# Kernel optimization log

Measured on AMD Instinct MI355X. Metric: run time of the kernel, lower is better.

Reference implementation:

```python
import jax, jax.numpy as jnp
import numpy as np

B, M, D, OUT = 16384, 4096, 512, 128


def setup_inputs() -> dict:
    key = jax.random.key(0)
    ks = jax.random.split(key, 5)
    x = jax.random.normal(ks[0], (B, D), dtype=jnp.float32)
    support = jax.random.normal(ks[1], (M, D), dtype=jnp.float32)
    gamma = jnp.float32(1.0)
    head_w = jax.random.normal(ks[2], (OUT, M), dtype=jnp.float32) / np.sqrt(M)
    head_b = jax.random.normal(ks[3], (OUT,), dtype=jnp.float32) * 0.01
    scale = jnp.ones((1,), dtype=jnp.float32)
    shift = jnp.zeros((1,), dtype=jnp.float32)
    return {"x": x, "support": support, "gamma": gamma,
            "head_w": head_w, "head_b": head_b,
            "scale": scale, "shift": shift}


def reference(x, support, gamma, head_w, head_b, scale, shift):
    x2 = jnp.sum(x * x, axis=-1, keepdims=True)           # [B, 1]
    s2 = jnp.sum(support * support, axis=-1)              # [M]
    xs = jnp.einsum('bd,md->bm', x, support)              # [B, M]
    sqdist = jnp.maximum(x2 + s2[None, :] - 2.0 * xs, 0.0)
    k = jnp.exp(-gamma * sqdist)                          # RBF kernel [B, M]
    out = jnp.einsum('bm,om->bo', k, head_w) + head_b     # linear head [B, OUT]
    return scale * out + shift
```

## Files before the change

### kernel.cpp

```cpp
#include <hip/hip_runtime.h>

typedef unsigned int u32;
typedef unsigned short u16;
typedef unsigned char u8;
typedef __attribute__((ext_vector_type(8))) __bf16 bf16x8;
typedef __attribute__((ext_vector_type(4))) float f32x4;
typedef __attribute__((ext_vector_type(4))) int i32x4;

#define NB 16384
#define NM 4096
#define ND 512
#define NOUT 128
#define L2E 1.44269504088896340736f


#define WAITLG(N) do { asm volatile("s_waitcnt vmcnt(" #N ") lgkmcnt(0)" ::: "memory"); \
                       __builtin_amdgcn_sched_barrier(0); } while (0)
#define LGKM(N) do { asm volatile("s_waitcnt lgkmcnt(" #N ")" ::: "memory"); \
                     __builtin_amdgcn_sched_barrier(0); } while (0)
#define SB0() __builtin_amdgcn_sched_barrier(0)

__device__ __forceinline__ u16 f2bf(float f) {
  u32 u = __float_as_uint(f);
  u += 0x7FFFu + ((u >> 16) & 1u);
  return (u16)(u >> 16);
}

__device__ __forceinline__ u8 f2fp8(float f) {
  u32 u = __float_as_uint(f);
  u32 s = (u >> 24) & 0x80u;
  u32 au = u & 0x7FFFFFFFu;
  if (au < 0x3C800000u) return (u8)s;
  au += 0x000FFFFFu + ((au >> 20) & 1u);
  u32 e = (au >> 23) - 120u;
  u32 m = (au >> 20) & 7u;
  return (u8)(s | (e << 3) | m);
}

__device__ __forceinline__ void stage16(const void* g, void* l) {
  __builtin_amdgcn_global_load_lds((__attribute__((address_space(1))) void*)g,
                                   (__attribute__((address_space(3))) void*)l,
                                   16, 0, 0);
}

__device__ __forceinline__ bf16x8 ldg_b128(const void* p) {
  i32x4 r;
  asm volatile("global_load_dwordx4 %0, %1, off" : "=&v"(r) : "v"(p) : "memory");
  return __builtin_bit_cast(bf16x8, r);
}

__device__ __forceinline__ uint4 pack8bf(float4 v0, float4 v1) {
  uint4 pk;
  pk.x = (u32)f2bf(v0.x) | ((u32)f2bf(v0.y) << 16);
  pk.y = (u32)f2bf(v0.z) | ((u32)f2bf(v0.w) << 16);
  pk.z = (u32)f2bf(v1.x) | ((u32)f2bf(v1.y) << 16);
  pk.w = (u32)f2bf(v1.z) | ((u32)f2bf(v1.w) << 16);
  return pk;
}

__device__ __forceinline__ uint2 pack8f8(float4 v0, float4 v1) {
  uint2 pk;
  pk.x = (u32)f2fp8(v0.x) | ((u32)f2fp8(v0.y) << 8) |
         ((u32)f2fp8(v0.z) << 16) | ((u32)f2fp8(v0.w) << 24);
  pk.y = (u32)f2fp8(v1.x) | ((u32)f2fp8(v1.y) << 8) |
         ((u32)f2fp8(v1.z) << 16) | ((u32)f2fp8(v1.w) << 24);
  return pk;
}

__global__ __launch_bounds__(256) void prep_all(const float* __restrict__ x,
                                                const float* __restrict__ s,
                                                const float* __restrict__ hw,
                                                const float* __restrict__ gamma_p,
                                                u8*  __restrict__ x_ws,
                                                u8*  __restrict__ s_ws,
                                                u16* __restrict__ hw_ws,
                                                float* __restrict__ x2g,
                                                float* __restrict__ s2g,
                                                float* __restrict__ out) {
  __shared__ uint2 t8[2048];
  __shared__ uint4 t16[2048];
  const int tid = threadIdx.x, bid = blockIdx.x;
  const int lane = tid & 63, w = tid >> 6;

  if (bid < 640) {
    const bool isx = bid < 512;
    const int blk = isx ? bid : (bid - 512);
    const float* src_m = isx ? x : s;
    u8*    dst_ws = isx ? x_ws : s_ws;
    float* sq_out = isx ? x2g : s2g;
    const float gl   = gamma_p[0] * L2E;
    const float cmul = isx ? 1.0f : (-2.0f * gl);
    const int big  = isx ? (blk >> 1) : (blk >> 2);
    const int roff = isx ? ((blk & 1) * 32) : ((blk & 3) * 32);
    const int rows = isx ? 64 : 128;

    #pragma unroll
    for (int p = 0; p < 8; ++p) {
      const int row = p * 4 + w;
      const float* src = src_m + (size_t)(blk * 32 + row) * ND + lane * 8;
      float4 v0 = *(const float4*)src;
      float4 v1 = *(const float4*)(src + 4);
      float ss = v0.x*v0.x + v0.y*v0.y + v0.z*v0.z + v0.w*v0.w
               + v1.x*v1.x + v1.y*v1.y + v1.z*v1.z + v1.w*v1.w;
      #pragma unroll
      for (int off = 32; off > 0; off >>= 1) ss += __shfl_down(ss, off);
      if (lane == 0) sq_out[blk * 32 + row] = gl * ss;
      v0.x *= cmul; v0.y *= cmul; v0.z *= cmul; v0.w *= cmul;
      v1.x *= cmul; v1.y *= cmul; v1.z *= cmul; v1.w *= cmul;
      t8[lane * 32 + ((row + lane) & 31)] = pack8f8(v0, v1);
    }
    __syncthreads();
    #pragma unroll
    for (int p = 0; p < 8; ++p) {
      const int kg = p * 8 + (tid >> 5);
      const int row = tid & 31;
      uint2 pk = t8[kg * 32 + ((row + kg) & 31)];
      *(uint2*)&dst_ws[(((size_t)(big * 64 + kg)) * rows + roff + row) * 8] = pk;
    }
  } else if (bid < 672) {
    const int blk = bid - 640;
    #pragma unroll
    for (int p = 0; p < 8; ++p) {
      const int o = p * 16 + (tid >> 4);
      const int kg = tid & 15;
      const float* src = hw + (size_t)o * NM + blk * 128 + kg * 8;
      float4 v0 = *(const float4*)src;
      float4 v1 = *(const float4*)(src + 4);
      t16[o * 16 + ((kg + o) & 15)] = pack8bf(v0, v1);
    }
    __syncthreads();
    #pragma unroll
    for (int it = 0; it < 8; ++it) {
      const int kg = it * 2 + (tid >> 7);
      const int o = tid & 127;
      uint4 pk = t16[o * 16 + ((kg + o) & 15)];
      *(uint4*)&hw_ws[(((size_t)(blk * 16 + kg)) * 128 + o) * 8] = pk;
    }
  } else {
    float4* o4 = (float4*)out;
    const float4 z = {0.f, 0.f, 0.f, 0.f};
    size_t base = (size_t)(bid - 672) * 8192 + tid;
    #pragma unroll 8
    for (int i = 0; i < 32; ++i) o4[base + (size_t)i * 256] = z;
  }
}

__global__ __launch_bounds__(256, 2)
void rbf_fused(const u8* __restrict__ x_ws, const u8* __restrict__ s_ws,
               const u16* __restrict__ hw_ws, const float* __restrict__ x2g,
               const float* __restrict__ s2g, const float* __restrict__ head_b,
               const float* __restrict__ scale_p, const float* __restrict__ shift_p,
               float* __restrict__ out)
{
  extern __shared__ __align__(16) char smem[];

  const int tid  = threadIdx.x;
  const int w    = tid >> 6;
  const int lane = tid & 63;
  const int quad = lane >> 4;
  const int l16  = lane & 15;
  const int wr   = w & 1;
  const int wc   = w >> 1;
  const int xcd  = blockIdx.x & 7;
  const int rb   = (blockIdx.x >> 3) * 2 + (xcd & 1);
  const int half = xcd >> 1;
  const int b0   = rb * 64;

  const float vscale = scale_p[0];
  const float vshift = shift_p[0];

  const u8* xsrc = x_ws + (size_t)rb * 32768;
  const u8* ssrc = s_ws + (size_t)(half * 8) * 65536;

  auto stage_grp = [&](int mt_s, int grp_s) {
    const u8* sp = ssrc + (size_t)mt_s * 65536 + grp_s * 8192;
    char* dp = smem + 32768 + (grp_s & 3) * 8192;
    stage16(sp + tid * 16, dp + tid * 16);
    stage16(sp + 4096 + tid * 16, dp + 4096 + tid * 16);
  };

  f32x4 x2v[2];
  #pragma unroll
  for (int r = 0; r < 2; ++r)
    x2v[r] = *(const f32x4*)&x2g[b0 + wr * 32 + r * 16 + quad * 4];
  SB0();
  #pragma unroll
  for (int i = 0; i < 8; ++i)
    stage16(xsrc + i * 4096 + tid * 16, smem + i * 4096 + tid * 16);
  SB0();
  stage_grp(0, 0); SB0();
  stage_grp(0, 1); SB0();
  stage_grp(0, 2);
  WAITLG(0);
  __builtin_amdgcn_s_barrier();
  SB0();

  long long aF[2][2][2];
  long long bF[2][2][4];
  bf16x8 b2[2][4];
  bf16x8 a2h[4][2];

  #pragma unroll
  for (int k2 = 0; k2 < 2; ++k2) {
    #pragma unroll
    for (int r = 0; r < 2; ++r)
      aF[0][k2][r] = *(const long long*)(smem + ((k2 * 4 + quad) * 64 + wr * 32 + r * 16 + l16) * 8);
    #pragma unroll
    for (int c = 0; c < 4; ++c)
      bF[0][k2][c] = *(const long long*)(smem + 32768 +
                       ((k2 * 4 + quad) * 128 + wc * 64 + c * 16 + l16) * 8);
  }
  LGKM(0);
  __builtin_amdgcn_s_barrier();
  SB0();

  const f32x4 zf = {0.f, 0.f, 0.f, 0.f};
  f32x4 acc_xs[2][4];
  f32x4 acc_out[2][4];
  #pragma unroll
  for (int r = 0; r < 2; ++r)
    #pragma unroll
    for (int c = 0; c < 4; ++c) { acc_xs[r][c] = zf; acc_out[r][c] = zf; }

  #pragma unroll 1
  for (int mt = 0; mt < 8; ++mt) {
    const int mtg = half * 8 + mt;

    if (mt > 0) {
      #pragma unroll
      for (int ks = 0; ks < 4; ++ks) {
        const int kg = ks * 4 + quad;
        #pragma unroll
        for (int r = 0; r < 2; ++r)
          a2h[ks][r] = *(const bf16x8*)(smem + 65536 + (kg * 64 + wr * 32 + r * 16 + l16) * 16);
      }
      LGKM(0);
    }
    float s2v[4];

    #pragma unroll
    for (int grp = 0; grp < 8; ++grp) {
      const int p  = grp & 1;
      const int pn = p ^ 1;
      const int gN = grp + 1;
      const bool doRd = !(mt == 7 && grp == 7);

      if ((grp & 1) == 0) {
        if (grp == 0) {
          #pragma unroll
          for (int c = 0; c < 4; ++c)
            s2v[c] = s2g[mtg * 128 + wc * 64 + c * 16 + l16];
          SB0();
        }
        if (grp == 0)      { stage_grp(mt, 3); stage_grp(mt, 4); }
        else if (grp == 2) { stage_grp(mt, 5); stage_grp(mt, 6); }
        else if (grp == 4) { stage_grp(mt, 7); if (mt < 7) stage_grp(mt + 1, 0); }
        else               { if (mt < 7) { stage_grp(mt + 1, 1); stage_grp(mt + 1, 2); } }
        SB0();
        if ((grp < 6 && mt >= 1) || (grp == 6 && mt <= 6)) {
          const int um = mt + (grp == 6);
          const int ks = ((grp >> 1) + 1) & 3;
          const size_t sb = (size_t)((half * 8 + um - 1) * 16 + ks * 4 + quad);
          #pragma unroll
          for (int c = 0; c < 4; ++c)
            b2[((grp >> 1) + 1) & 1][c] = ldg_b128(hw_ws + (sb * 128 + wc * 64 + c * 16 + l16) * 8);
        }
        SB0();
      }

      __builtin_amdgcn_s_setprio(1);
      #pragma unroll
      for (int r = 0; r < 2; ++r)
        #pragma unroll
        for (int c = 0; c < 4; ++c)
          acc_xs[r][c] = __builtin_amdgcn_mfma_f32_16x16x32_fp8_fp8(
              aF[p][0][r], bF[p][0][c], acc_xs[r][c], 0, 0, 0);
      __builtin_amdgcn_s_setprio(0);
      SB0();
      if (doRd) {
        #pragma unroll
        for (int k2 = 0; k2 < 2; ++k2)
          #pragma unroll
          for (int r = 0; r < 2; ++r)
            aF[pn][k2][r] = *(const long long*)(smem +
                ((((gN & 7) * 2 + k2) * 4 + quad) * 64 + wr * 32 + r * 16 + l16) * 8);
        #pragma unroll
        for (int c = 0; c < 2; ++c)
          bF[pn][0][c] = *(const long long*)(smem + 32768 + (gN & 3) * 8192 +
              ((0 * 4 + quad) * 128 + wc * 64 + c * 16 + l16) * 8);
      }
      SB0();

      __builtin_amdgcn_s_setprio(1);
      #pragma unroll
      for (int r = 0; r < 2; ++r)
        #pragma unroll
        for (int c = 0; c < 4; ++c)
          acc_xs[r][c] = __builtin_amdgcn_mfma_f32_16x16x32_fp8_fp8(
              aF[p][1][r], bF[p][1][c], acc_xs[r][c], 0, 0, 0);
      __builtin_amdgcn_s_setprio(0);
      SB0();
      if (doRd) {
        #pragma unroll
        for (int c = 2; c < 4; ++c)
          bF[pn][0][c] = *(const long long*)(smem + 32768 + (gN & 3) * 8192 +
              ((0 * 4 + quad) * 128 + wc * 64 + c * 16 + l16) * 8);
        #pragma unroll
        for (int c = 0; c < 4; ++c)
          bF[pn][1][c] = *(const long long*)(smem + 32768 + (gN & 3) * 8192 +
              ((1 * 4 + quad) * 128 + wc * 64 + c * 16 + l16) * 8);
      }
      SB0();

      if ((grp & 1) == 0) {
        if (mt > 0) {
          __builtin_amdgcn_s_setprio(1);
          #pragma unroll
          for (int r = 0; r < 2; ++r)
            #pragma unroll
            for (int c = 0; c < 4; ++c)
              acc_out[r][c] = __builtin_amdgcn_mfma_f32_16x16x32_bf16(
                  a2h[grp >> 1][r], b2[(grp >> 1) & 1][c], acc_out[r][c], 0, 0, 0);
          __builtin_amdgcn_s_setprio(0);
        }
        LGKM(0);
      } else {
        WAITLG(0);
        __builtin_amdgcn_s_barrier();
        SB0();
      }
    }

    {
      #pragma unroll
      for (int r = 0; r < 2; ++r)
        #pragma unroll
        for (int c = 0; c < 4; ++c) {
          const int cl = wc * 64 + c * 16 + l16;
          char* kbase = smem + 65536 + (cl >> 3) * 1024 + (cl & 7) * 2;
          #pragma unroll
          for (int i = 0; i < 4; ++i) {
            const int row = wr * 32 + r * 16 + quad * 4 + i;
            const float t = acc_xs[r][c][i] + x2v[r][i] + s2v[c];
            float kv = __builtin_amdgcn_exp2f(-t);
            kv = fminf(kv, 1.0f);
            *(u16*)(kbase + row * 16) = (u16)(__float_as_uint(kv) >> 16);
            acc_xs[r][c][i] = 0.0f;
          }
        }
    }
    LGKM(0);
    __builtin_amdgcn_s_barrier();
    SB0();
  }

  #pragma unroll
  for (int ks = 0; ks < 4; ++ks) {
    const int kg = ks * 4 + quad;
    const size_t sb = (size_t)((half * 8 + 7) * 16 + kg);
    bf16x8 bb[4], aa[2];
    #pragma unroll
    for (int c = 0; c < 4; ++c)
      bb[c] = *(const bf16x8*)(hw_ws + (sb * 128 + wc * 64 + c * 16 + l16) * 8);
    #pragma unroll
    for (int r = 0; r < 2; ++r)
      aa[r] = *(const bf16x8*)(smem + 65536 + (kg * 64 + wr * 32 + r * 16 + l16) * 16);
    #pragma unroll
    for (int r = 0; r < 2; ++r)
      #pragma unroll
      for (int c = 0; c < 4; ++c)
        acc_out[r][c] = __builtin_amdgcn_mfma_f32_16x16x32_bf16(aa[r], bb[c], acc_out[r][c], 0, 0, 0);
  }

  float addv[4];
  #pragma unroll
  for (int c = 0; c < 4; ++c) {
    const int col = wc * 64 + c * 16 + l16;
    addv[c] = (half == 0) ? (vscale * head_b[col] + vshift) : 0.0f;
  }
  #pragma unroll
  for (int r = 0; r < 2; ++r)
    #pragma unroll
    for (int c = 0; c < 4; ++c) {
      const int col = wc * 64 + c * 16 + l16;
      #pragma unroll
      for (int i = 0; i < 4; ++i) {
        const int row = b0 + wr * 32 + r * 16 + quad * 4 + i;
        atomicAdd(&out[(size_t)row * NOUT + col], vscale * acc_out[r][c][i] + addv[c]);
      }
    }
}

extern "C" void kernel_launch(void* const* d_in, const int* in_sizes, int n_in,
                              void* d_out, int out_size, void* d_ws, size_t ws_size,
                              hipStream_t stream) {
  const float* x       = (const float*)d_in[0];
  const float* support = (const float*)d_in[1];
  const float* gamma   = (const float*)d_in[2];
  const float* head_w  = (const float*)d_in[3];
  const float* head_b  = (const float*)d_in[4];
  const float* scale   = (const float*)d_in[5];
  const float* shift   = (const float*)d_in[6];
  float* out = (float*)d_out;

  char* w = (char*)d_ws;
  u8*    x_ws  = (u8*)(w);
  u8*    s_ws  = (u8*)(w + 8388608);
  u16*   hw_ws = (u16*)(w + 10485760);
  float* x2g   = (float*)(w + 11534336);
  float* s2g   = (float*)(w + 11599872);

  static bool lds_init = false;
  if (!lds_init) {
    hipFuncSetAttribute(reinterpret_cast<const void*>(rbf_fused),
                        hipFuncAttributeMaxDynamicSharedMemorySize, 81920);
    lds_init = true;
  }

  prep_all<<<736, 256, 0, stream>>>(x, support, head_w, gamma,
                                    x_ws, s_ws, hw_ws, x2g, s2g, out);
  rbf_fused<<<1024, 256, 81920, stream>>>(x_ws, s_ws, hw_ws, x2g, s2g,
                                          head_b, scale, shift, out);
}
```

Measured before the change: 182.3 us.

## Load x fragments straight from global and shrink LDS to static 48KB

The x tile is no longer staged into LDS. Each wave loads its fp8 A fragments directly from global memory with dwordx2 loads, one group ahead. LDS drops from 80KB dynamic to 48KB static, which could allow more blocks per CU. Support staging now runs one group per iteration, the per-tile bulk read of the kernel matrix is split into per-step reads, and the waitcnt and barrier schedule is retuned to match. The cost is more global load traffic and latency exposed in the inner loop.

Measured after the change: 243.8 us. 1.34x slower.

```diff
diff --git a/kernel.cpp b/kernel.cpp
--- a/kernel.cpp
+++ b/kernel.cpp
@@ -47,6 +47,11 @@
   i32x4 r;
   asm volatile("global_load_dwordx4 %0, %1, off" : "=&v"(r) : "v"(p) : "memory");
   return __builtin_bit_cast(bf16x8, r);
+}
+__device__ __forceinline__ long long ldg_b64(const void* p) {
+  long long r;
+  asm volatile("global_load_dwordx2 %0, %1, off" : "=&v"(r) : "v"(p) : "memory");
+  return r;
 }
 
 __device__ __forceinline__ uint4 pack8bf(float4 v0, float4 v1) {
@@ -152,7 +157,7 @@
                const float* __restrict__ scale_p, const float* __restrict__ shift_p,
                float* __restrict__ out)
 {
-  extern __shared__ __align__(16) char smem[];
+  __shared__ __align__(16) char smem[49152];
 
   const int tid  = threadIdx.x;
   const int w    = tid >> 6;
@@ -172,44 +177,43 @@
   const u8* xsrc = x_ws + (size_t)rb * 32768;
   const u8* ssrc = s_ws + (size_t)(half * 8) * 65536;
 
+  const u8* xb0 = xsrc + quad * 512 + (wr * 32 + l16) * 8;
+  const u8* xb1 = xsrc + quad * 512 + (wr * 32 + 16 + l16) * 8;
+
   auto stage_grp = [&](int mt_s, int grp_s) {
     const u8* sp = ssrc + (size_t)mt_s * 65536 + grp_s * 8192;
-    char* dp = smem + 32768 + (grp_s & 3) * 8192;
+    char* dp = smem + (grp_s & 3) * 8192;
     stage16(sp + tid * 16, dp + tid * 16);
     stage16(sp + 4096 + tid * 16, dp + 4096 + tid * 16);
   };
 
+  long long aF[2][2][2];
+  long long bF[2][2][4];
+  bf16x8 b2[2][4];
+  bf16x8 a2[2];
+
   f32x4 x2v[2];
   #pragma unroll
   for (int r = 0; r < 2; ++r)
     x2v[r] = *(const f32x4*)&x2g[b0 + wr * 32 + r * 16 + quad * 4];
   SB0();
-  #pragma unroll
-  for (int i = 0; i < 8; ++i)
-    stage16(xsrc + i * 4096 + tid * 16, smem + i * 4096 + tid * 16);
-  SB0();
   stage_grp(0, 0); SB0();
   stage_grp(0, 1); SB0();
-  stage_grp(0, 2);
+  stage_grp(0, 2); SB0();
+  aF[0][0][0] = ldg_b64(xb0);
+  aF[0][0][1] = ldg_b64(xb1);
+  aF[0][1][0] = ldg_b64(xb0 + 2048);
+  aF[0][1][1] = ldg_b64(xb1 + 2048);
   WAITLG(0);
   __builtin_amdgcn_s_barrier();
   SB0();
 
-  long long aF[2][2][2];
-  long long bF[2][2][4];
-  bf16x8 b2[2][4];
-  bf16x8 a2h[4][2];
-
-  #pragma unroll
-  for (int k2 = 0; k2 < 2; ++k2) {
-    #pragma unroll
-    for (int r = 0; r < 2; ++r)
-      aF[0][k2][r] = *(const long long*)(smem + ((k2 * 4 + quad) * 64 + wr * 32 + r * 16 + l16) * 8);
+  #pragma unroll
+  for (int k2 = 0; k2 < 2; ++k2)
     #pragma unroll
     for (int c = 0; c < 4; ++c)
-      bF[0][k2][c] = *(const long long*)(smem + 32768 +
+      bF[0][k2][c] = *(const long long*)(smem +
                        ((k2 * 4 + quad) * 128 + wc * 64 + c * 16 + l16) * 8);
-  }
   LGKM(0);
   __builtin_amdgcn_s_barrier();
   SB0();
@@ -225,17 +229,6 @@
   #pragma unroll 1
   for (int mt = 0; mt < 8; ++mt) {
     const int mtg = half * 8 + mt;
-
-    if (mt > 0) {
-      #pragma unroll
-      for (int ks = 0; ks < 4; ++ks) {
-        const int kg = ks * 4 + quad;
-        #pragma unroll
-        for (int r = 0; r < 2; ++r)
-          a2h[ks][r] = *(const bf16x8*)(smem + 65536 + (kg * 64 + wr * 32 + r * 16 + l16) * 16);
-      }
-      LGKM(0);
-    }
     float s2v[4];
 
     #pragma unroll
@@ -245,28 +238,32 @@
       const int gN = grp + 1;
       const bool doRd = !(mt == 7 && grp == 7);
 
-      if ((grp & 1) == 0) {
-        if (grp == 0) {
-          #pragma unroll
-          for (int c = 0; c < 4; ++c)
-            s2v[c] = s2g[mtg * 128 + wc * 64 + c * 16 + l16];
-          SB0();
-        }
-        if (grp == 0)      { stage_grp(mt, 3); stage_grp(mt, 4); }
-        else if (grp == 2) { stage_grp(mt, 5); stage_grp(mt, 6); }
-        else if (grp == 4) { stage_grp(mt, 7); if (mt < 7) stage_grp(mt + 1, 0); }
-        else               { if (mt < 7) { stage_grp(mt + 1, 1); stage_grp(mt + 1, 2); } }
+      if (grp == 0) {
+        #pragma unroll
+        for (int c = 0; c < 4; ++c)
+          s2v[c] = s2g[mtg * 128 + wc * 64 + c * 16 + l16];
         SB0();
-        if ((grp < 6 && mt >= 1) || (grp == 6 && mt <= 6)) {
-          const int um = mt + (grp == 6);
-          const int ks = ((grp >> 1) + 1) & 3;
-          const size_t sb = (size_t)((half * 8 + um - 1) * 16 + ks * 4 + quad);
-          #pragma unroll
-          for (int c = 0; c < 4; ++c)
-            b2[((grp >> 1) + 1) & 1][c] = ldg_b128(hw_ws + (sb * 128 + wc * 64 + c * 16 + l16) * 8);
-        }
-        SB0();
-      }
+      }
+      if (doRd) {
+        const int xo = (gN & 7) * 4096;
+        aF[pn][0][0] = ldg_b64(xb0 + xo);
+        aF[pn][0][1] = ldg_b64(xb1 + xo);
+        aF[pn][1][0] = ldg_b64(xb0 + xo + 2048);
+        aF[pn][1][1] = ldg_b64(xb1 + xo + 2048);
+      }
+      SB0();
+      if (grp <= 4)     stage_grp(mt, grp + 3);
+      else if (mt < 7)  stage_grp(mt + 1, grp - 5);
+      SB0();
+      if ((grp & 1) == 0 && ((grp < 6 && mt >= 1) || (grp == 6 && mt <= 6))) {
+        const int um = mt + (grp == 6);
+        const int ks = ((grp >> 1) + 1) & 3;
+        const size_t sb = (size_t)((half * 8 + um - 1) * 16 + ks * 4 + quad);
+        #pragma unroll
+        for (int c = 0; c < 4; ++c)
+          b2[((grp >> 1) + 1) & 1][c] = ldg_b128(hw_ws + (sb * 128 + wc * 64 + c * 16 + l16) * 8);
+      }
+      SB0();
 
       __builtin_amdgcn_s_setprio(1);
       #pragma unroll
@@ -279,15 +276,15 @@
       SB0();
       if (doRd) {
         #pragma unroll
-        for (int k2 = 0; k2 < 2; ++k2)
-          #pragma unroll
-          for (int r = 0; r < 2; ++r)
-            aF[pn][k2][r] = *(const long long*)(smem +
-                ((((gN & 7) * 2 + k2) * 4 + quad) * 64 + wr * 32 + r * 16 + l16) * 8);
-        #pragma unroll
-        for (int c = 0; c < 2; ++c)
-          bF[pn][0][c] = *(const long long*)(smem + 32768 + (gN & 3) * 8192 +
+        for (int c = 0; c < 4; ++c)
+          bF[pn][0][c] = *(const long long*)(smem + (gN & 3) * 8192 +
               ((0 * 4 + quad) * 128 + wc * 64 + c * 16 + l16) * 8);
+      }
+      if (mt > 0 && (grp & 1) == 0) {
+        const int kg = (grp >> 1) * 4 + quad;
+        #pragma unroll
+        for (int r = 0; r < 2; ++r)
+          a2[r] = *(const bf16x8*)(smem + 32768 + (kg * 64 + wr * 32 + r * 16 + l16) * 16);
       }
       SB0();
 
@@ -302,33 +299,33 @@
       SB0();
       if (doRd) {
         #pragma unroll
-        for (int c = 2; c < 4; ++c)
-          bF[pn][0][c] = *(const long long*)(smem + 32768 + (gN & 3) * 8192 +
-              ((0 * 4 + quad) * 128 + wc * 64 + c * 16 + l16) * 8);
-        #pragma unroll
-        for (int c = 0; c < 4; ++c)
-          bF[pn][1][c] = *(const long long*)(smem + 32768 + (gN & 3) * 8192 +
+        for (int c = 0; c < 4; ++c)
+          bF[pn][1][c] = *(const long long*)(smem + (gN & 3) * 8192 +
               ((1 * 4 + quad) * 128 + wc * 64 + c * 16 + l16) * 8);
       }
       SB0();
 
-      if ((grp & 1) == 0) {
-        if (mt > 0) {
-          __builtin_amdgcn_s_setprio(1);
+      if (mt > 0 && (grp & 1) == 0) {
+        __builtin_amdgcn_s_setprio(1);
+        #pragma unroll
+        for (int r = 0; r < 2; ++r)
           #pragma unroll
-          for (int r = 0; r < 2; ++r)
-            #pragma unroll
-            for (int c = 0; c < 4; ++c)
-              acc_out[r][c] = __builtin_amdgcn_mfma_f32_16x16x32_bf16(
-                  a2h[grp >> 1][r], b2[(grp >> 1) & 1][c], acc_out[r][c], 0, 0, 0);
-          __builtin_amdgcn_s_setprio(0);
-        }
-        LGKM(0);
-      } else {
-        WAITLG(0);
-        __builtin_amdgcn_s_barrier();
-        SB0();
-      }
+          for (int c = 0; c < 4; ++c)
+            acc_out[r][c] = __builtin_amdgcn_mfma_f32_16x16x32_bf16(
+                a2[r], b2[(grp >> 1) & 1][c], acc_out[r][c], 0, 0, 0);
+        __builtin_amdgcn_s_setprio(0);
+      }
+      SB0();
+
+      if (mt == 0)      { if (grp == 6) WAITLG(6); else WAITLG(2); }
+      else if (mt < 7)  { if ((grp & 1) == 0) WAITLG(6); else WAITLG(2); }
+      else {
+        if (grp == 0 || grp == 2 || grp == 4)      WAITLG(6);
+        else if (grp == 1 || grp == 3)             WAITLG(2);
+        else                                       WAITLG(0);
+      }
+      __builtin_amdgcn_s_barrier();
+      SB0();
     }
 
     {
@@ -337,7 +334,7 @@
         #pragma unroll
         for (int c = 0; c < 4; ++c) {
           const int cl = wc * 64 + c * 16 + l16;
-          char* kbase = smem + 65536 + (cl >> 3) * 1024 + (cl & 7) * 2;
+          char* kbase = smem + 32768 + (cl >> 3) * 1024 + (cl & 7) * 2;
           #pragma unroll
           for (int i = 0; i < 4; ++i) {
             const int row = wr * 32 + r * 16 + quad * 4 + i;
@@ -364,7 +361,7 @@
       bb[c] = *(const bf16x8*)(hw_ws + (sb * 128 + wc * 64 + c * 16 + l16) * 8);
     #pragma unroll
     for (int r = 0; r < 2; ++r)
-      aa[r] = *(const bf16x8*)(smem + 65536 + (kg * 64 + wr * 32 + r * 16 + l16) * 16);
+      aa[r] = *(const bf16x8*)(smem + 32768 + (kg * 64 + wr * 32 + r * 16 + l16) * 16);
     #pragma unroll
     for (int r = 0; r < 2; ++r)
       #pragma unroll
@@ -410,15 +407,8 @@
   float* x2g   = (float*)(w + 11534336);
   float* s2g   = (float*)(w + 11599872);
 
-  static bool lds_init = false;
-  if (!lds_init) {
-    hipFuncSetAttribute(reinterpret_cast<const void*>(rbf_fused),
-                        hipFuncAttributeMaxDynamicSharedMemorySize, 81920);
-    lds_init = true;
-  }
-
   prep_all<<<736, 256, 0, stream>>>(x, support, head_w, gamma,
                                     x_ws, s_ws, hw_ws, x2g, s2g, out);
-  rbf_fused<<<1024, 256, 81920, stream>>>(x_ws, s_ws, hw_ws, x2g, s2g,
-                                          head_b, scale, shift, out);
-}
+  rbf_fused<<<1024, 256, 0, stream>>>(x_ws, s_ws, hw_ws, x2g, s2g,
+                                      head_b, scale, shift, out);
+}
```
